# Kernel optimization log

Hardware: AMD Instinct MI355X
Metric: run time of the kernel (lower is better)

## Reference

```python
import jax, jax.numpy as jnp
import numpy as np

N_NODES = 50000
N_EDGES = 800000
D_IN, D_HID, D_OUT = 128, 256, 256


def _sage_conv(x, src, dst, w_l, b_l, w_r, n_nodes):
    # PyG SAGEConv (mean aggr): out = lin_l(mean_{j in N(i)} x_j) + lin_r(x_i)
    # lin_l has bias, lin_r has no bias.
    msg_sum = jax.ops.segment_sum(x[src], dst, num_segments=n_nodes)  # [N, d]
    deg = jax.ops.segment_sum(jnp.ones_like(dst, dtype=x.dtype), dst, num_segments=n_nodes)
    agg = msg_sum / jnp.maximum(deg, 1.0)[:, None]
    return agg @ w_l.T + b_l + x @ w_r.T


def setup_inputs() -> dict:
    key = jax.random.key(0)
    ks = jax.random.split(key, 8)
    x = jax.random.normal(ks[0], (N_NODES, D_IN), dtype=jnp.float32)
    edge_index = jax.random.randint(ks[1], (2, N_EDGES), 0, N_NODES, dtype=jnp.int64)
    s1 = 1.0 / np.sqrt(D_IN)
    s2 = 1.0 / np.sqrt(D_HID)
    w_l1 = jax.random.uniform(ks[2], (D_HID, D_IN), jnp.float32, -s1, s1)
    b_l1 = jax.random.uniform(ks[3], (D_HID,), jnp.float32, -s1, s1)
    w_r1 = jax.random.uniform(ks[4], (D_HID, D_IN), jnp.float32, -s1, s1)
    w_l2 = jax.random.uniform(ks[5], (D_OUT, D_HID), jnp.float32, -s2, s2)
    b_l2 = jax.random.uniform(ks[6], (D_OUT,), jnp.float32, -s2, s2)
    w_r2 = jax.random.uniform(ks[7], (D_OUT, D_HID), jnp.float32, -s2, s2)
    return {"x": x, "edge_index": edge_index,
            "w_l1": w_l1, "b_l1": b_l1, "w_r1": w_r1,
            "w_l2": w_l2, "b_l2": b_l2, "w_r2": w_r2}


def reference(x, edge_index, w_l1, b_l1, w_r1, w_l2, b_l2, w_r2):
    src, dst = edge_index[0], edge_index[1]
    h = jax.nn.relu(_sage_conv(x, src, dst, w_l1, b_l1, w_r1, N_NODES))
    out = jax.nn.relu(_sage_conv(h, src, dst, w_l2, b_l2, w_r2, N_NODES))
    return out
```

## Files before the change

### kernel.cpp

```cpp
#include <hip/hip_runtime.h>
#include <stdint.h>

#define N_NODES 50000
#define N_EDGES 800000
#define BCAP 64
#define NPART 782
#define NSUB 4
#define SCAP 384

typedef __attribute__((ext_vector_type(8))) short bf16x8;
typedef __attribute__((ext_vector_type(4))) float f32x4;

__device__ __forceinline__ float bf2f(unsigned short u) {
    return __builtin_bit_cast(float, (unsigned int)u << 16);
}
__device__ __forceinline__ unsigned short f2bf(float f) {
    unsigned int u = __builtin_bit_cast(unsigned int, f);
    u += 0x7fffu + ((u >> 16) & 1u);
    return (unsigned short)(u >> 16);
}

__device__ __forceinline__ unsigned char f2fp8(float f) {
    f = fminf(f, 448.f);
    if (f < 0.015625f) {
        return (unsigned char)(int)__builtin_rintf(f * 512.f);
    }
    unsigned int u = __builtin_bit_cast(unsigned int, f);
    u += 0x7FFFFu + ((u >> 20) & 1u);
    return (unsigned char)((u >> 20) - 960u);
}
__device__ __forceinline__ void accf8x4(float* a, unsigned int w) {
#pragma unroll
    for (int b = 0; b < 4; b++) {
        unsigned int c = (w >> (8 * b)) & 0xFFu;
        float n = __builtin_bit_cast(float, 0x3C000000u + (c << 20));
        a[b] += (c < 8u) ? (float)c * 0.001953125f : n;
    }
}

__device__ __forceinline__ void load_lds16(const void* g, void* l) {
    __builtin_amdgcn_global_load_lds(
        (const __attribute__((address_space(1))) void*)(uintptr_t)g,
        (__attribute__((address_space(3))) void*)(unsigned int)(uintptr_t)l,
        16, 0, 0);
}

__global__ __launch_bounds__(256) void part_append_k(
    const int* __restrict__ src, const int* __restrict__ dst,
    int* __restrict__ pcnt, unsigned int* __restrict__ pbuf, int nedges)
{
    int e = blockIdx.x * 256 + threadIdx.x;
    if (e >= nedges) return;
    int s = src[e], d = dst[e];
    int cidx = (d >> 6) * NSUB + (e & (NSUB - 1));
    int pos = atomicAdd(&pcnt[cidx * 16], 1);
    if (pos < SCAP)
        pbuf[(size_t)cidx * SCAP + pos] = ((unsigned)(d & 63) << 16) | (unsigned)s;
}

__global__ __launch_bounds__(256) void part_bucket_k(
    const int* __restrict__ pcnt, const unsigned int* __restrict__ pbuf,
    int* __restrict__ bucket, int* __restrict__ degtot, float* __restrict__ invdeg)
{
    __shared__ int lcnt[64];
    int part = blockIdx.x, tid = threadIdx.x;
    if (tid < 64) lcnt[tid] = 0;
    __syncthreads();
#pragma unroll
    for (int sub = 0; sub < NSUB; sub++) {
        int cidx = part * NSUB + sub;
        int n = pcnt[cidx * 16];
        if (n > SCAP) n = SCAP;
        const unsigned int* pb = pbuf + (size_t)cidx * SCAP;
        for (int i = tid; i < n; i += 256) {
            unsigned int en = pb[i];
            int dlow = (int)(en >> 16), s = (int)(en & 0xFFFFu);
            int p = atomicAdd(&lcnt[dlow], 1);
            if (p < BCAP) bucket[(size_t)(part * 64 + dlow) * BCAP + p] = s;
        }
    }
    __syncthreads();
    if (tid < 64) {
        int node = part * 64 + tid;
        if (node < N_NODES) {
            int c = lcnt[tid];
            degtot[node] = (c > BCAP) ? BCAP : c;
            invdeg[node] = 1.0f / (float)(c > 1 ? c : 1);
        }
    }
}

__global__ __launch_bounds__(256) void cvt_x_k(
    const float* __restrict__ x, unsigned short* __restrict__ dst)
{
    int tid = blockIdx.x * 256 + threadIdx.x;
    if (tid >= N_NODES * 32) return;
    int row = tid >> 5, c = (tid & 31) * 4;
    float4 v = *(const float4*)(x + (size_t)row * 128 + c);
    ushort4 o;
    o.x = f2bf(v.x); o.y = f2bf(v.y); o.z = f2bf(v.z); o.w = f2bf(v.w);
    *(ushort4*)(dst + (size_t)row * 256 + 128 + c) = o;
}

__global__ __launch_bounds__(256) void cvt_w_k(
    const float* __restrict__ wl, const float* __restrict__ wr,
    unsigned short* __restrict__ dst, int Keach)
{
    int tid = blockIdx.x * 256 + threadIdx.x;
    if (tid >= 256 * 2 * Keach) return;
    int n = tid / (2 * Keach), k = tid - n * 2 * Keach;
    float v = (k < Keach) ? wl[(size_t)n * Keach + k]
                          : wr[(size_t)n * Keach + (k - Keach)];
    dst[tid] = f2bf(v);
}

__device__ __forceinline__ void acc8(float* a, uint4 u) {
    a[0] += bf2f((unsigned short)u.x); a[1] += bf2f((unsigned short)(u.x >> 16));
    a[2] += bf2f((unsigned short)u.y); a[3] += bf2f((unsigned short)(u.y >> 16));
    a[4] += bf2f((unsigned short)u.z); a[5] += bf2f((unsigned short)(u.z >> 16));
    a[6] += bf2f((unsigned short)u.w); a[7] += bf2f((unsigned short)(u.w >> 16));
}

__global__ __launch_bounds__(256) void agg1_k(
    const unsigned short* __restrict__ feat,
    const int* __restrict__ bucket, const int* __restrict__ degtot,
    const float* __restrict__ invdeg,
    unsigned short* __restrict__ outmsg)
{
    int wv = threadIdx.x >> 6, lane = threadIdx.x & 63;
    int node = blockIdx.x * 4 + wv;
    if (node >= N_NODES) return;
    int deg = degtot[node];
    int idx0 = bucket[(size_t)node * BCAP + lane];
    const int sub = lane >> 4;
    const int col = lane & 15;

    float acc[8] = {};
    auto rowp = [&](int s) { return (const uint4*)(feat + (size_t)s * 256 + col * 8); };

    int j = 0;
    for (; j + 16 <= deg; j += 16) {
        int s0 = __shfl(idx0, j + sub),     s1 = __shfl(idx0, j + 4 + sub);
        int s2 = __shfl(idx0, j + 8 + sub), s3 = __shfl(idx0, j + 12 + sub);
        uint4 u0 = *rowp(s0), u1 = *rowp(s1), u2 = *rowp(s2), u3 = *rowp(s3);
        acc8(acc, u0); acc8(acc, u1); acc8(acc, u2); acc8(acc, u3);
    }
    for (; j + 8 <= deg; j += 8) {
        int s0 = __shfl(idx0, j + sub), s1 = __shfl(idx0, j + 4 + sub);
        uint4 u0 = *rowp(s0), u1 = *rowp(s1);
        acc8(acc, u0); acc8(acc, u1);
    }
    for (; j + 4 <= deg; j += 4) {
        uint4 u0 = *rowp(__shfl(idx0, j + sub));
        acc8(acc, u0);
    }
    if (j < deg) {
        int e = j + sub;
        int ec = (e < deg) ? e : (deg - 1);
        uint4 u0 = *rowp(__shfl(idx0, ec));
        if (e < deg) acc8(acc, u0);
    }
#pragma unroll
    for (int stride = 32; stride >= 16; stride >>= 1)
#pragma unroll
        for (int v = 0; v < 8; v++) acc[v] += __shfl_xor(acc[v], stride);

    if (lane < 16) {
        float s = invdeg[node];
        uint4 o;
        o.x = (unsigned int)f2bf(acc[0] * s) | ((unsigned int)f2bf(acc[1] * s) << 16);
        o.y = (unsigned int)f2bf(acc[2] * s) | ((unsigned int)f2bf(acc[3] * s) << 16);
        o.z = (unsigned int)f2bf(acc[4] * s) | ((unsigned int)f2bf(acc[5] * s) << 16);
        o.w = (unsigned int)f2bf(acc[6] * s) | ((unsigned int)f2bf(acc[7] * s) << 16);
        *(uint4*)(outmsg + (size_t)node * 256 + lane * 8) = o;
    }
}

__device__ __forceinline__ void acc16f8(float* a, uint4 u) {
    accf8x4(a + 0, u.x); accf8x4(a + 4, u.y); accf8x4(a + 8, u.z); accf8x4(a + 12, u.w);
}

__global__ __launch_bounds__(256) void agg2_k(
    const unsigned char* __restrict__ hf8,
    const int* __restrict__ bucket, const int* __restrict__ degtot,
    const float* __restrict__ invdeg,
    unsigned short* __restrict__ outmsg)
{
    int wv = threadIdx.x >> 6, lane = threadIdx.x & 63;
    int node = blockIdx.x * 4 + wv;
    if (node >= N_NODES) return;
    int deg = degtot[node];
    int idx0 = bucket[(size_t)node * BCAP + lane];
    const int sub = lane >> 4;
    const int col = lane & 15;

    float acc[16] = {};
    auto rowp = [&](int s) { return (const uint4*)(hf8 + (size_t)s * 256 + col * 16); };

    int j = 0;
    for (; j + 16 <= deg; j += 16) {
        int s0 = __shfl(idx0, j + sub),     s1 = __shfl(idx0, j + 4 + sub);
        int s2 = __shfl(idx0, j + 8 + sub), s3 = __shfl(idx0, j + 12 + sub);
        uint4 u0 = *rowp(s0), u1 = *rowp(s1), u2 = *rowp(s2), u3 = *rowp(s3);
        acc16f8(acc, u0); acc16f8(acc, u1); acc16f8(acc, u2); acc16f8(acc, u3);
    }
    for (; j + 8 <= deg; j += 8) {
        int s0 = __shfl(idx0, j + sub), s1 = __shfl(idx0, j + 4 + sub);
        uint4 u0 = *rowp(s0), u1 = *rowp(s1);
        acc16f8(acc, u0); acc16f8(acc, u1);
    }
    for (; j + 4 <= deg; j += 4) {
        uint4 u0 = *rowp(__shfl(idx0, j + sub));
        acc16f8(acc, u0);
    }
    if (j < deg) {
        int e = j + sub;
        int ec = (e < deg) ? e : (deg - 1);
        uint4 u0 = *rowp(__shfl(idx0, ec));
        if (e < deg) acc16f8(acc, u0);
    }
#pragma unroll
    for (int stride = 32; stride >= 16; stride >>= 1)
#pragma unroll
        for (int v = 0; v < 16; v++) acc[v] += __shfl_xor(acc[v], stride);

    if (lane < 16) {
        float s = invdeg[node];
        unsigned int o[8];
#pragma unroll
        for (int v = 0; v < 8; v++)
            o[v] = (unsigned int)f2bf(acc[2 * v] * s) | ((unsigned int)f2bf(acc[2 * v + 1] * s) << 16);
        unsigned short* wp = outmsg + (size_t)node * 512 + lane * 16;
        *(uint4*)(wp)     = make_uint4(o[0], o[1], o[2], o[3]);
        *(uint4*)(wp + 8) = make_uint4(o[4], o[5], o[6], o[7]);
    }
}

template <bool BF16OUT, bool WRITE_FP8>
__global__ __launch_bounds__(256) void gemm_k(
    const unsigned short* __restrict__ A, const unsigned short* __restrict__ W,
    const float* __restrict__ bias, void* __restrict__ outp, int outStride,
    unsigned char* __restrict__ hf8, int M, int K)
{
    __shared__ __align__(16) char smem[(128 + 128) * 64];
    const int t = threadIdx.x;
    const int w = t >> 6, lane = t & 63;
    const int quad = lane >> 4, l15 = lane & 15;
    const int row0 = blockIdx.x * 128;
    const int col0 = blockIdx.y * 128;

    f32x4 acc[2][8] = {};

    for (int ks = 0; ks < K; ks += 32) {
#pragma unroll
        for (int j = 0; j < 4; j++) {
            int call = w * 4 + j;
            int ci = call * 64 + lane;
            const unsigned short* g;
            if (call < 8) {
                int rg = row0 + (ci >> 2);
                if (rg > M - 1) rg = M - 1;
                g = A + (size_t)rg * K + ks + (ci & 3) * 8;
            } else {
                int c2 = ci - 512;
                g = W + (size_t)(col0 + (c2 >> 2)) * K + ks + (c2 & 3) * 8;
            }
            load_lds16(g, smem + ci * 16);
        }
        __syncthreads();

        const char* Ab = smem + (w * 32 + l15) * 64 + quad * 16;
        const char* Wb = smem + 8192 + l15 * 64 + quad * 16;
        bf16x8 af0 = *(const bf16x8*)(Ab);
        bf16x8 af1 = *(const bf16x8*)(Ab + 1024);
#pragma unroll
        for (int tt = 0; tt < 8; tt++) {
            bf16x8 bfr = *(const bf16x8*)(Wb + tt * 1024);
            acc[0][tt] = __builtin_amdgcn_mfma_f32_16x16x32_bf16(af0, bfr, acc[0][tt], 0, 0, 0);
            acc[1][tt] = __builtin_amdgcn_mfma_f32_16x16x32_bf16(af1, bfr, acc[1][tt], 0, 0, 0);
        }
        __syncthreads();
    }

#pragma unroll
    for (int g = 0; g < 2; g++) {
#pragma unroll
        for (int tt = 0; tt < 8; tt++) {
            int col = col0 + tt * 16 + l15;
            float bv = bias[col];
#pragma unroll
            for (int i = 0; i < 4; i++) {
                int row = row0 + w * 32 + g * 16 + quad * 4 + i;
                if (row < M) {
                    float v = fmaxf(acc[g][tt][i] + bv, 0.f);
                    size_t off = (size_t)row * outStride + col;
                    if constexpr (BF16OUT) ((unsigned short*)outp)[off] = f2bf(v);
                    else                   ((float*)outp)[off] = v;
                    if constexpr (WRITE_FP8) hf8[(size_t)row * 256 + col] = f2fp8(v);
                }
            }
        }
    }
}

extern "C" void kernel_launch(void* const* d_in, const int* in_sizes, int n_in,
                              void* d_out, int out_size, void* d_ws, size_t ws_size,
                              hipStream_t stream)
{
    const float* x   = (const float*)d_in[0];
    const int*   ei  = (const int*)d_in[1];
    const float* wl1 = (const float*)d_in[2];
    const float* bl1 = (const float*)d_in[3];
    const float* wr1 = (const float*)d_in[4];
    const float* wl2 = (const float*)d_in[5];
    const float* bl2 = (const float*)d_in[6];
    const float* wr2 = (const float*)d_in[7];
    float* out = (float*)d_out;
    const int* src = ei;
    const int* dst = ei + N_EDGES;

    char* ws = (char*)d_ws;
    size_t off = 0;
    auto alloc = [&](size_t bytes) -> void* {
        void* p = ws + off;
        off = (off + bytes + 255) & ~(size_t)255;
        return p;
    };
    int*            pcnt   = (int*)           alloc((size_t)NPART * NSUB * 16 * 4);
    unsigned int*   pbuf   = (unsigned int*)  alloc((size_t)NPART * NSUB * SCAP * 4);
    int*            bucket = (int*)           alloc((size_t)NPART * 64 * BCAP * 4);
    int*            degtot = (int*)           alloc((size_t)N_NODES * 4);
    float*          invdeg = (float*)         alloc((size_t)N_NODES * 4);
    unsigned short* Acat1  = (unsigned short*)alloc((size_t)N_NODES * 256 * 2);
    unsigned short* Acat2  = (unsigned short*)alloc((size_t)N_NODES * 512 * 2);
    unsigned char*  hf8    = (unsigned char*) alloc((size_t)N_NODES * 256);
    unsigned short* Wcat1  = (unsigned short*)alloc((size_t)256 * 256 * 2);
    unsigned short* Wcat2  = (unsigned short*)alloc((size_t)256 * 512 * 2);

    hipMemsetAsync(pcnt, 0, (size_t)NPART * NSUB * 16 * 4, stream);
    part_append_k<<<(N_EDGES + 255) / 256, 256, 0, stream>>>(src, dst, pcnt, pbuf, N_EDGES);
    part_bucket_k<<<NPART, 256, 0, stream>>>(pcnt, pbuf, bucket, degtot, invdeg);

    cvt_x_k<<<(N_NODES * 32 + 255) / 256, 256, 0, stream>>>(x, Acat1);
    cvt_w_k<<<(256 * 256 + 255) / 256, 256, 0, stream>>>(wl1, wr1, Wcat1, 128);
    cvt_w_k<<<(256 * 512 + 255) / 256, 256, 0, stream>>>(wl2, wr2, Wcat2, 256);

    agg1_k<<<(N_NODES + 3) / 4, 256, 0, stream>>>(
        Acat1 + 128, bucket, degtot, invdeg, Acat1);
    gemm_k<true, true><<<dim3((N_NODES + 127) / 128, 2), 256, 0, stream>>>(
        Acat1, Wcat1, bl1, (void*)(Acat2 + 256), 512, hf8, N_NODES, 256);

    agg2_k<<<(N_NODES + 3) / 4, 256, 0, stream>>>(
        hf8, bucket, degtot, invdeg, Acat2);
    gemm_k<false, false><<<dim3((N_NODES + 127) / 128, 2), 256, 0, stream>>>(
        Acat2, Wcat2, bl2, (void*)out, 256, nullptr, N_NODES, 512);
}
```

Before: 318.6 us.

## Switch aggregation and GEMM from bf16 to fp16 with packed half2 accumulation

Replaces bf16 storage and MFMA with fp16, and accumulates neighbor sums in packed __half2 instead of scalar fp32. The layer-2 fp8 encoding gains an offset so bytes can be decoded into fp16 with shifts, masks and adds, two values per instruction, and the offset is subtracted after the mean. This cuts ALU work in the gather loops, which were dominated by per-element conversion and fp32 adds. The cost is reduced accuracy: fp16 accumulation over up to 64 neighbors can lose precision and the range is narrower than bf16.

```diff
diff --git a/kernel.cpp b/kernel.cpp
--- a/kernel.cpp
+++ b/kernel.cpp
@@ -1,4 +1,5 @@
 #include <hip/hip_runtime.h>
+#include <hip/hip_fp16.h>
 #include <stdint.h>
 
 #define N_NODES 50000
@@ -8,34 +9,18 @@
 #define NSUB 4
 #define SCAP 384
 
-typedef __attribute__((ext_vector_type(8))) short bf16x8;
+typedef _Float16 f16x8 __attribute__((ext_vector_type(8)));
 typedef __attribute__((ext_vector_type(4))) float f32x4;
 
-__device__ __forceinline__ float bf2f(unsigned short u) {
-    return __builtin_bit_cast(float, (unsigned int)u << 16);
-}
-__device__ __forceinline__ unsigned short f2bf(float f) {
-    unsigned int u = __builtin_bit_cast(unsigned int, f);
-    u += 0x7fffu + ((u >> 16) & 1u);
-    return (unsigned short)(u >> 16);
-}
-
-__device__ __forceinline__ unsigned char f2fp8(float f) {
-    f = fminf(f, 448.f);
-    if (f < 0.015625f) {
-        return (unsigned char)(int)__builtin_rintf(f * 512.f);
-    }
-    unsigned int u = __builtin_bit_cast(unsigned int, f);
+__device__ __forceinline__ unsigned short f2h(float f) {
+    return __builtin_bit_cast(unsigned short, (_Float16)f);
+}
+
+__device__ __forceinline__ unsigned char f2fp8o(float v) {
+    v = fminf(v, 440.f) + 0.015625f;
+    unsigned int u = __builtin_bit_cast(unsigned int, v);
     u += 0x7FFFFu + ((u >> 20) & 1u);
     return (unsigned char)((u >> 20) - 960u);
-}
-__device__ __forceinline__ void accf8x4(float* a, unsigned int w) {
-#pragma unroll
-    for (int b = 0; b < 4; b++) {
-        unsigned int c = (w >> (8 * b)) & 0xFFu;
-        float n = __builtin_bit_cast(float, 0x3C000000u + (c << 20));
-        a[b] += (c < 8u) ? (float)c * 0.001953125f : n;
-    }
 }
 
 __device__ __forceinline__ void load_lds16(const void* g, void* l) {
@@ -98,7 +83,7 @@
     int row = tid >> 5, c = (tid & 31) * 4;
     float4 v = *(const float4*)(x + (size_t)row * 128 + c);
     ushort4 o;
-    o.x = f2bf(v.x); o.y = f2bf(v.y); o.z = f2bf(v.z); o.w = f2bf(v.w);
+    o.x = f2h(v.x); o.y = f2h(v.y); o.z = f2h(v.z); o.w = f2h(v.w);
     *(ushort4*)(dst + (size_t)row * 256 + 128 + c) = o;
 }
 
@@ -111,14 +96,14 @@
     int n = tid / (2 * Keach), k = tid - n * 2 * Keach;
     float v = (k < Keach) ? wl[(size_t)n * Keach + k]
                           : wr[(size_t)n * Keach + (k - Keach)];
-    dst[tid] = f2bf(v);
-}
-
-__device__ __forceinline__ void acc8(float* a, uint4 u) {
-    a[0] += bf2f((unsigned short)u.x); a[1] += bf2f((unsigned short)(u.x >> 16));
-    a[2] += bf2f((unsigned short)u.y); a[3] += bf2f((unsigned short)(u.y >> 16));
-    a[4] += bf2f((unsigned short)u.z); a[5] += bf2f((unsigned short)(u.z >> 16));
-    a[6] += bf2f((unsigned short)u.w); a[7] += bf2f((unsigned short)(u.w >> 16));
+    dst[tid] = f2h(v);
+}
+
+__device__ __forceinline__ void acch4(__half2* a, uint4 u) {
+    a[0] = __hadd2(a[0], __builtin_bit_cast(__half2, u.x));
+    a[1] = __hadd2(a[1], __builtin_bit_cast(__half2, u.y));
+    a[2] = __hadd2(a[2], __builtin_bit_cast(__half2, u.z));
+    a[3] = __hadd2(a[3], __builtin_bit_cast(__half2, u.w));
 }
 
 __global__ __launch_bounds__(256) void agg1_k(
@@ -135,7 +120,7 @@
     const int sub = lane >> 4;
     const int col = lane & 15;
 
-    float acc[8] = {};
+    __half2 acc[4] = {};
     auto rowp = [&](int s) { return (const uint4*)(feat + (size_t)s * 256 + col * 8); };
 
     int j = 0;
@@ -143,41 +128,51 @@
         int s0 = __shfl(idx0, j + sub),     s1 = __shfl(idx0, j + 4 + sub);
         int s2 = __shfl(idx0, j + 8 + sub), s3 = __shfl(idx0, j + 12 + sub);
         uint4 u0 = *rowp(s0), u1 = *rowp(s1), u2 = *rowp(s2), u3 = *rowp(s3);
-        acc8(acc, u0); acc8(acc, u1); acc8(acc, u2); acc8(acc, u3);
+        acch4(acc, u0); acch4(acc, u1); acch4(acc, u2); acch4(acc, u3);
     }
     for (; j + 8 <= deg; j += 8) {
         int s0 = __shfl(idx0, j + sub), s1 = __shfl(idx0, j + 4 + sub);
         uint4 u0 = *rowp(s0), u1 = *rowp(s1);
-        acc8(acc, u0); acc8(acc, u1);
+        acch4(acc, u0); acch4(acc, u1);
     }
     for (; j + 4 <= deg; j += 4) {
         uint4 u0 = *rowp(__shfl(idx0, j + sub));
-        acc8(acc, u0);
+        acch4(acc, u0);
     }
     if (j < deg) {
         int e = j + sub;
         int ec = (e < deg) ? e : (deg - 1);
         uint4 u0 = *rowp(__shfl(idx0, ec));
-        if (e < deg) acc8(acc, u0);
+        if (e < deg) acch4(acc, u0);
     }
 #pragma unroll
     for (int stride = 32; stride >= 16; stride >>= 1)
 #pragma unroll
-        for (int v = 0; v < 8; v++) acc[v] += __shfl_xor(acc[v], stride);
+        for (int v = 0; v < 4; v++) {
+            int t = __shfl_xor(__builtin_bit_cast(int, acc[v]), stride);
+            acc[v] = __hadd2(acc[v], __builtin_bit_cast(__half2, t));
+        }
 
     if (lane < 16) {
         float s = invdeg[node];
-        uint4 o;
-        o.x = (unsigned int)f2bf(acc[0] * s) | ((unsigned int)f2bf(acc[1] * s) << 16);
-        o.y = (unsigned int)f2bf(acc[2] * s) | ((unsigned int)f2bf(acc[3] * s) << 16);
-        o.z = (unsigned int)f2bf(acc[4] * s) | ((unsigned int)f2bf(acc[5] * s) << 16);
-        o.w = (unsigned int)f2bf(acc[6] * s) | ((unsigned int)f2bf(acc[7] * s) << 16);
-        *(uint4*)(outmsg + (size_t)node * 256 + lane * 8) = o;
-    }
-}
-
-__device__ __forceinline__ void acc16f8(float* a, uint4 u) {
-    accf8x4(a + 0, u.x); accf8x4(a + 4, u.y); accf8x4(a + 8, u.z); accf8x4(a + 12, u.w);
+        unsigned int o[4];
+#pragma unroll
+        for (int v = 0; v < 4; v++) {
+            float2 f = __half22float2(acc[v]);
+            o[v] = (unsigned int)f2h(f.x * s) | ((unsigned int)f2h(f.y * s) << 16);
+        }
+        *(uint4*)(outmsg + (size_t)node * 256 + lane * 8) = make_uint4(o[0], o[1], o[2], o[3]);
+    }
+}
+
+__device__ __forceinline__ void accf8pk(__half2* a, unsigned int w) {
+    unsigned int ev = ((w & 0x00FF00FFu) << 7) + 0x20002000u;
+    unsigned int od = ((w >> 1) & 0x7F807F80u) + 0x20002000u;
+    a[0] = __hadd2(a[0], __builtin_bit_cast(__half2, ev));
+    a[1] = __hadd2(a[1], __builtin_bit_cast(__half2, od));
+}
+__device__ __forceinline__ void accf8x16(__half2* a, uint4 u) {
+    accf8pk(a + 0, u.x); accf8pk(a + 2, u.y); accf8pk(a + 4, u.z); accf8pk(a + 6, u.w);
 }
 
 __global__ __launch_bounds__(256) void agg2_k(
@@ -194,7 +189,7 @@
     const int sub = lane >> 4;
     const int col = lane & 15;
 
-    float acc[16] = {};
+    __half2 acc[8] = {};
     auto rowp = [&](int s) { return (const uint4*)(hf8 + (size_t)s * 256 + col * 16); };
 
     int j = 0;
@@ -202,41 +197,51 @@
         int s0 = __shfl(idx0, j + sub),     s1 = __shfl(idx0, j + 4 + sub);
         int s2 = __shfl(idx0, j + 8 + sub), s3 = __shfl(idx0, j + 12 + sub);
         uint4 u0 = *rowp(s0), u1 = *rowp(s1), u2 = *rowp(s2), u3 = *rowp(s3);
-        acc16f8(acc, u0); acc16f8(acc, u1); acc16f8(acc, u2); acc16f8(acc, u3);
+        accf8x16(acc, u0); accf8x16(acc, u1); accf8x16(acc, u2); accf8x16(acc, u3);
     }
     for (; j + 8 <= deg; j += 8) {
         int s0 = __shfl(idx0, j + sub), s1 = __shfl(idx0, j + 4 + sub);
         uint4 u0 = *rowp(s0), u1 = *rowp(s1);
-        acc16f8(acc, u0); acc16f8(acc, u1);
+        accf8x16(acc, u0); accf8x16(acc, u1);
     }
     for (; j + 4 <= deg; j += 4) {
         uint4 u0 = *rowp(__shfl(idx0, j + sub));
-        acc16f8(acc, u0);
+        accf8x16(acc, u0);
     }
     if (j < deg) {
         int e = j + sub;
         int ec = (e < deg) ? e : (deg - 1);
         uint4 u0 = *rowp(__shfl(idx0, ec));
-        if (e < deg) acc16f8(acc, u0);
+        if (e < deg) accf8x16(acc, u0);
     }
 #pragma unroll
     for (int stride = 32; stride >= 16; stride >>= 1)
 #pragma unroll
-        for (int v = 0; v < 16; v++) acc[v] += __shfl_xor(acc[v], stride);
+        for (int v = 0; v < 8; v++) {
+            int t = __shfl_xor(__builtin_bit_cast(int, acc[v]), stride);
+            acc[v] = __hadd2(acc[v], __builtin_bit_cast(__half2, t));
+        }
 
     if (lane < 16) {
         float s = invdeg[node];
+        float bias = (deg > 0) ? 0.015625f : 0.0f;
         unsigned int o[8];
 #pragma unroll
-        for (int v = 0; v < 8; v++)
-            o[v] = (unsigned int)f2bf(acc[2 * v] * s) | ((unsigned int)f2bf(acc[2 * v + 1] * s) << 16);
+        for (int q = 0; q < 4; q++) {
+            float2 ev = __half22float2(acc[2 * q]);
+            float2 od = __half22float2(acc[2 * q + 1]);
+            float d0 = ev.x * s - bias, d1 = od.x * s - bias;
+            float d2 = ev.y * s - bias, d3 = od.y * s - bias;
+            o[2 * q]     = (unsigned int)f2h(d0) | ((unsigned int)f2h(d1) << 16);
+            o[2 * q + 1] = (unsigned int)f2h(d2) | ((unsigned int)f2h(d3) << 16);
+        }
         unsigned short* wp = outmsg + (size_t)node * 512 + lane * 16;
         *(uint4*)(wp)     = make_uint4(o[0], o[1], o[2], o[3]);
         *(uint4*)(wp + 8) = make_uint4(o[4], o[5], o[6], o[7]);
     }
 }
 
-template <bool BF16OUT, bool WRITE_FP8>
+template <bool F16OUT, bool WRITE_FP8>
 __global__ __launch_bounds__(256) void gemm_k(
     const unsigned short* __restrict__ A, const unsigned short* __restrict__ W,
     const float* __restrict__ bias, void* __restrict__ outp, int outStride,
@@ -271,13 +276,13 @@
 
         const char* Ab = smem + (w * 32 + l15) * 64 + quad * 16;
         const char* Wb = smem + 8192 + l15 * 64 + quad * 16;
-        bf16x8 af0 = *(const bf16x8*)(Ab);
-        bf16x8 af1 = *(const bf16x8*)(Ab + 1024);
+        f16x8 af0 = *(const f16x8*)(Ab);
+        f16x8 af1 = *(const f16x8*)(Ab + 1024);
 #pragma unroll
         for (int tt = 0; tt < 8; tt++) {
-            bf16x8 bfr = *(const bf16x8*)(Wb + tt * 1024);
-            acc[0][tt] = __builtin_amdgcn_mfma_f32_16x16x32_bf16(af0, bfr, acc[0][tt], 0, 0, 0);
-            acc[1][tt] = __builtin_amdgcn_mfma_f32_16x16x32_bf16(af1, bfr, acc[1][tt], 0, 0, 0);
+            f16x8 bfr = *(const f16x8*)(Wb + tt * 1024);
+            acc[0][tt] = __builtin_amdgcn_mfma_f32_16x16x32_f16(af0, bfr, acc[0][tt], 0, 0, 0);
+            acc[1][tt] = __builtin_amdgcn_mfma_f32_16x16x32_f16(af1, bfr, acc[1][tt], 0, 0, 0);
         }
         __syncthreads();
     }
@@ -294,9 +299,9 @@
                 if (row < M) {
                     float v = fmaxf(acc[g][tt][i] + bv, 0.f);
                     size_t off = (size_t)row * outStride + col;
-                    if constexpr (BF16OUT) ((unsigned short*)outp)[off] = f2bf(v);
-                    else                   ((float*)outp)[off] = v;
-                    if constexpr (WRITE_FP8) hf8[(size_t)row * 256 + col] = f2fp8(v);
+                    if constexpr (F16OUT) ((unsigned short*)outp)[off] = f2h(v);
+                    else                  ((float*)outp)[off] = v;
+                    if constexpr (WRITE_FP8) hf8[(size_t)row * 256 + col] = f2fp8o(v);
                 }
             }
         }
```

Result: faster. 288.2 us (-9.6%).
